# Kernel tuning notes

Hardware: AMD Instinct MI355X
Metric: run time of the kernel (lower is better)

Reference implementation:

```python
import jax, jax.numpy as jnp
import numpy as np

EMBED = 1024
HEADS = 16

def setup_inputs() -> dict:
    key = jax.random.key(0)
    ks = jax.random.split(key, 6)
    N, S = 1, 4096
    half = EMBED // 2
    x = jax.random.normal(ks[0], (N, S, EMBED), dtype=jnp.float32)
    Wq = jax.random.normal(ks[1], (half, half), dtype=jnp.float32) * 0.02
    Wk = jax.random.normal(ks[2], (half, half), dtype=jnp.float32) * 0.02
    Wv = jax.random.normal(ks[3], (half, half), dtype=jnp.float32) * 0.02
    Wo = jax.random.normal(ks[4], (EMBED, half), dtype=jnp.float32) * 0.02
    bo = jnp.zeros((EMBED,), dtype=jnp.float32)
    return {"x": x, "Wq": Wq, "Wk": Wk, "Wv": Wv, "Wo": Wo, "bo": bo}

def reference(x, Wq, Wk, Wv, Wo, bo):
    N, S, E = x.shape
    H = HEADS
    Dh = (E // 2) // H                 # per-head dim of the half-width projections (32)
    scale = float(E // H) ** 0.5       # original scales by head_dim = embed/heads = 64
    left = x[..., : E // 2]            # only the left chunk feeds attention in the source
    # torch Linear: y = x @ W.T (no bias)
    q = (left @ Wq.T).reshape(N, S, H, Dh)
    k = (left @ Wk.T).reshape(N, S, H, Dh)
    v = (left @ Wv.T).reshape(N, S, H, Dh)
    energy = jnp.einsum('nqhd,nkhd->nqkh', q, k)          # [N,S,S,H] full score tensor
    att = jax.nn.softmax(energy / scale, axis=2)          # softmax over key axis
    out = jnp.einsum('nqkh,nkhd->nqhd', att, v)           # [N,S,H,Dh]
    out = out.reshape(N, S, E // 2)
    return out @ Wo.T + bo                                # fc_out: half -> embed
```

## Files before the change

### kernel.cpp

```cpp
#include <hip/hip_runtime.h>
#include <stdint.h>


#define SEQ    4096
#define DMODEL 1024
#define DHALF  512
#define NH     16
#define DH     32

typedef __attribute__((ext_vector_type(4))) float facc4;
typedef __attribute__((ext_vector_type(8))) short bfrag8;

#define MFMA_BF16(a, b, c) __builtin_amdgcn_mfma_f32_16x16x32_bf16((a), (b), (c), 0, 0, 0)

static __device__ __forceinline__ uint16_t f2b(float x) {
    uint32_t u = __float_as_uint(x);
    return (uint16_t)((u + 0x7FFFu + ((u >> 16) & 1u)) >> 16);
}
static __device__ __forceinline__ float b2f(uint16_t b) {
    return __uint_as_float(((uint32_t)b) << 16);
}

static __device__ __forceinline__ bfrag8 cvt8perm(float4 a, float4 b) {
    uint32_t u0 = __float_as_uint(a.x) + 0x8000u, u1 = __float_as_uint(a.y) + 0x8000u;
    uint32_t u2 = __float_as_uint(a.z) + 0x8000u, u3 = __float_as_uint(a.w) + 0x8000u;
    uint32_t u4 = __float_as_uint(b.x) + 0x8000u, u5 = __float_as_uint(b.y) + 0x8000u;
    uint32_t u6 = __float_as_uint(b.z) + 0x8000u, u7 = __float_as_uint(b.w) + 0x8000u;
    union { uint32_t w[4]; bfrag8 r; } u;
    u.w[0] = __builtin_amdgcn_perm(u1, u0, 0x07060302u);
    u.w[1] = __builtin_amdgcn_perm(u3, u2, 0x07060302u);
    u.w[2] = __builtin_amdgcn_perm(u5, u4, 0x07060302u);
    u.w[3] = __builtin_amdgcn_perm(u7, u6, 0x07060302u);
    return u.r;
}

__global__ __launch_bounds__(256) void convert_w(
    const float* __restrict__ Wq, const float* __restrict__ Wk,
    const float* __restrict__ Wv, const float* __restrict__ Wo,
    uint16_t* __restrict__ q, uint16_t* __restrict__ k,
    uint16_t* __restrict__ v, uint16_t* __restrict__ o)
{
    int zz = blockIdx.x;
    const float* src; uint16_t* dst; size_t off;
    if      (zz < 128) { src = Wq; dst = q; off = (size_t)zz * 2048; }
    else if (zz < 256) { src = Wk; dst = k; off = (size_t)(zz - 128) * 2048; }
    else if (zz < 384) { src = Wv; dst = v; off = (size_t)(zz - 256) * 2048; }
    else               { src = Wo; dst = o; off = (size_t)(zz - 384) * 2048; }
    size_t i = off + (size_t)threadIdx.x * 8;
    float4 a = *(const float4*)&src[i];
    float4 b = *(const float4*)&src[i + 4];
    *(bfrag8*)&dst[i] = cvt8perm(a, b);
}

template <int AF32>
__device__ __forceinline__ void gemm128T(
    const void* __restrict__ A, int lda,
    const uint16_t* __restrict__ B, int ldb,
    void* __restrict__ C, int ldc, int cF32,
    const float* __restrict__ bias, float scale,
    int Kd, int m0, int n0)
{
    __shared__ __align__(16) uint16_t As[2][128 * 40];
    __shared__ __align__(16) uint16_t Bs[2][128 * 40];

    const int tid  = threadIdx.x;
    const int lane = tid & 63;
    const int wv   = tid >> 6;
    const int lo   = lane & 15;
    const int quad = lane >> 4;
    const int srow = tid >> 2;
    const int skq  = (tid & 3) * 8;
    const int rb   = (wv >> 1) * 64;
    const int cb   = (wv & 1) * 64;

    const facc4 ZACC = {0.f, 0.f, 0.f, 0.f};
    facc4 acc[4][4];
#pragma unroll
    for (int i = 0; i < 4; ++i)
#pragma unroll
        for (int j = 0; j < 4; ++j) acc[i][j] = ZACC;

    const float*    fA0 = AF32 ? &((const float*)A)[(size_t)(m0 + srow) * lda + skq] : nullptr;
    const float*    fA1 = AF32 ? &((const float*)A)[(size_t)(m0 + srow + 64) * lda + skq] : nullptr;
    const uint16_t* hA0 = AF32 ? nullptr : &((const uint16_t*)A)[(size_t)(m0 + srow) * lda + skq];
    const uint16_t* hA1 = AF32 ? nullptr : &((const uint16_t*)A)[(size_t)(m0 + srow + 64) * lda + skq];
    const uint16_t* pB0 = &B[(size_t)(n0 + srow) * ldb + skq];
    const uint16_t* pB1 = &B[(size_t)(n0 + srow + 64) * ldb + skq];

    bfrag8 ra0, ra1;
    float4 f0a, f0b, f1a, f1b;
    if (AF32) {
        f0a = *(const float4*)fA0; f0b = *(const float4*)(fA0 + 4);
        f1a = *(const float4*)fA1; f1b = *(const float4*)(fA1 + 4);
    } else {
        ra0 = *(const bfrag8*)hA0;
        ra1 = *(const bfrag8*)hA1;
    }
    bfrag8 rb0 = *(const bfrag8*)pB0;
    bfrag8 rb1 = *(const bfrag8*)pB1;

    if (AF32) {
        *(bfrag8*)&As[0][srow * 40 + skq]        = cvt8perm(f0a, f0b);
        *(bfrag8*)&As[0][(srow + 64) * 40 + skq] = cvt8perm(f1a, f1b);
    } else {
        *(bfrag8*)&As[0][srow * 40 + skq]        = ra0;
        *(bfrag8*)&As[0][(srow + 64) * 40 + skq] = ra1;
    }
    *(bfrag8*)&Bs[0][srow * 40 + skq]        = rb0;
    *(bfrag8*)&Bs[0][(srow + 64) * 40 + skq] = rb1;
    __syncthreads();

    int p = 0;
    for (int kt = 0; kt < Kd; kt += 32) {
        const bool more = (kt + 32 < Kd);
        if (more) {
            if (AF32) {
                f0a = *(const float4*)(fA0 + kt + 32); f0b = *(const float4*)(fA0 + kt + 36);
                f1a = *(const float4*)(fA1 + kt + 32); f1b = *(const float4*)(fA1 + kt + 36);
            } else {
                ra0 = *(const bfrag8*)(hA0 + kt + 32);
                ra1 = *(const bfrag8*)(hA1 + kt + 32);
            }
            rb0 = *(const bfrag8*)(pB0 + kt + 32);
            rb1 = *(const bfrag8*)(pB1 + kt + 32);
        }

        bfrag8 af[4], bf[4];
#pragma unroll
        for (int i = 0; i < 4; ++i) {
            af[i] = *(const bfrag8*)&As[p][(rb + i * 16 + lo) * 40 + quad * 8];
            bf[i] = *(const bfrag8*)&Bs[p][(cb + i * 16 + lo) * 40 + quad * 8];
        }
#pragma unroll
        for (int i = 0; i < 4; ++i)
#pragma unroll
            for (int j = 0; j < 4; ++j)
                acc[i][j] = MFMA_BF16(af[i], bf[j], acc[i][j]);

        if (more) {
            if (AF32) {
                *(bfrag8*)&As[1 - p][srow * 40 + skq]        = cvt8perm(f0a, f0b);
                *(bfrag8*)&As[1 - p][(srow + 64) * 40 + skq] = cvt8perm(f1a, f1b);
            } else {
                *(bfrag8*)&As[1 - p][srow * 40 + skq]        = ra0;
                *(bfrag8*)&As[1 - p][(srow + 64) * 40 + skq] = ra1;
            }
            *(bfrag8*)&Bs[1 - p][srow * 40 + skq]        = rb0;
            *(bfrag8*)&Bs[1 - p][(srow + 64) * 40 + skq] = rb1;
            __syncthreads();
            p ^= 1;
        }
    }

#pragma unroll
    for (int j = 0; j < 4; ++j) {
        int col  = n0 + cb + j * 16 + lo;
        float bv = bias ? bias[col] : 0.f;
#pragma unroll
        for (int i = 0; i < 4; ++i) {
#pragma unroll
            for (int r = 0; r < 4; ++r) {
                int row = m0 + rb + i * 16 + quad * 4 + r;
                float v = acc[i][j][r] * scale + bv;
                if (cF32) ((float*)C)[(size_t)row * ldc + col] = v;
                else      ((uint16_t*)C)[(size_t)row * ldc + col] = f2b(v);
            }
        }
    }
}

#define SC_Q (0.125f * 1.4426950408889634f)

__global__ __launch_bounds__(256, 2) void qkv_kernel(
    const float* __restrict__ x,
    const uint16_t* __restrict__ Wqb, const uint16_t* __restrict__ Wkb,
    const uint16_t* __restrict__ Wvb,
    uint16_t* __restrict__ Q, uint16_t* __restrict__ K, uint16_t* __restrict__ V)
{
    const int z = blockIdx.z;
    const uint16_t* W = (z == 0) ? Wqb : (z == 1) ? Wkb : Wvb;
    uint16_t* Out     = (z == 0) ? Q   : (z == 1) ? K   : V;
    float scale       = (z == 0) ? SC_Q : 1.0f;
    gemm128T<1>(x, DMODEL, W, DHALF, Out, DHALF, 0, nullptr, scale, DHALF,
                blockIdx.y * 128, blockIdx.x * 128);
}

__global__ __launch_bounds__(256, 2) void outproj_kernel(
    const uint16_t* __restrict__ O, const uint16_t* __restrict__ Wob,
    const float* __restrict__ bo, float* __restrict__ Y)
{
    gemm128T<0>(O, DHALF, Wob, DHALF, Y, DMODEL, 1, bo, 1.0f, DHALF,
                blockIdx.y * 128, blockIdx.x * 128);
}

__global__ __launch_bounds__(256) void attn_kernel(
    const uint16_t* __restrict__ Q, const uint16_t* __restrict__ Kb,
    const uint16_t* __restrict__ Vb, uint16_t* __restrict__ Op,
    float* __restrict__ lbuf, int kspan)
{
    __shared__ __align__(16) uint16_t Ks[64 * 40];
    __shared__ __align__(16) uint16_t Vt[32 * 64];
    __shared__ __align__(16) uint16_t Ps[4 * 16 * 72];

    const int tid  = threadIdx.x;
    const int lane = tid & 63;
    const int wv   = tid >> 6;
    const int lo   = lane & 15;
    const int quad = lane >> 4;
    const int h    = blockIdx.y;
    const int q0   = blockIdx.x * 64;
    const int sp   = blockIdx.z;
    const int srow = tid >> 2;
    const int skq  = (tid & 3) * 8;

    const facc4 ZACC = {0.f, 0.f, 0.f, 0.f};

    const bfrag8 qf = *(const bfrag8*)&Q[(size_t)(q0 + wv * 16 + lo) * DHALF + h * DH + quad * 8];

    bfrag8 ones;
#pragma unroll
    for (int j = 0; j < 8; ++j) ones[j] = (short)0x3F80;

    int vt_w[8];
#pragma unroll
    for (int j = 0; j < 8; ++j) {
        int d  = skq + j;
        int Rd = ((d & 7) + 2 * (d >> 3)) & 7;
        vt_w[j] = d * 64 + ((((srow >> 3) + Rd) & 7) << 3) + (srow & 7);
    }
    int vt_r[2][2];
#pragma unroll
    for (int dt = 0; dt < 2; ++dt) {
        int d  = dt * 16 + lo;
        int Rd = ((d & 7) + 2 * (d >> 3)) & 7;
#pragma unroll
        for (int c = 0; c < 2; ++c)
            vt_r[c][dt] = d * 64 + ((((c * 4 + quad) + Rd) & 7) << 3);
    }
    const int pbase = wv * (16 * 72);
    const int ps_w  = pbase + lo * 72 + 4 * quad;
    const int ps_r  = pbase + lo * 72 + quad * 8;
    const int ks_r  = lo * 40 + quad * 8;

    const uint16_t* pK = &Kb[(size_t)srow * DHALF + h * DH + skq];
    const uint16_t* pV = &Vb[(size_t)srow * DHALF + h * DH + skq];

    facc4 oacc[2], oaccL;
    oacc[0] = ZACC; oacc[1] = ZACC; oaccL = ZACC;

    const int kb0  = sp * kspan;
    const int kend = kb0 + kspan;

    float4 kreg = *(const float4*)(pK + (size_t)kb0 * DHALF);
    float4 vreg = *(const float4*)(pV + (size_t)kb0 * DHALF);

    for (int kb = kb0; kb < kend; kb += 64) {
        *(float4*)&Ks[srow * 40 + skq] = kreg;
        {
            const uint16_t* vp = (const uint16_t*)&vreg;
#pragma unroll
            for (int j = 0; j < 8; ++j) Vt[vt_w[j]] = vp[j];
        }
        __syncthreads();

        if (kb + 64 < kend) {
            kreg = *(const float4*)(pK + (size_t)(kb + 64) * DHALF);
            vreg = *(const float4*)(pV + (size_t)(kb + 64) * DHALF);
        }

#pragma unroll
        for (int t = 0; t < 4; ++t) {
            bfrag8 kf = *(const bfrag8*)&Ks[t * 640 + ks_r];
            facc4 s = MFMA_BF16(kf, qf, ZACC);
            float p0 = __builtin_amdgcn_exp2f(s[0]);
            float p1 = __builtin_amdgcn_exp2f(s[1]);
            float p2 = __builtin_amdgcn_exp2f(s[2]);
            float p3 = __builtin_amdgcn_exp2f(s[3]);
            uint32_t u0 = __float_as_uint(p0) + 0x8000u;
            uint32_t u1 = __float_as_uint(p1) + 0x8000u;
            uint32_t u2 = __float_as_uint(p2) + 0x8000u;
            uint32_t u3 = __float_as_uint(p3) + 0x8000u;
            uint2 w;
            w.x = __builtin_amdgcn_perm(u1, u0, 0x07060302u);
            w.y = __builtin_amdgcn_perm(u3, u2, 0x07060302u);
            *(uint2*)&Ps[ps_w + 16 * t] = w;
        }
        __builtin_amdgcn_wave_barrier();

#pragma unroll
        for (int c = 0; c < 2; ++c) {
            bfrag8 pf = *(const bfrag8*)&Ps[ps_r + c * 32];
#pragma unroll
            for (int dt = 0; dt < 2; ++dt) {
                bfrag8 vf = *(const bfrag8*)&Vt[vt_r[c][dt]];
                oacc[dt] = MFMA_BF16(pf, vf, oacc[dt]);
            }
            oaccL = MFMA_BF16(pf, ones, oaccL);
        }
        __syncthreads();
    }

    if (lo == 0) {
#pragma unroll
        for (int r = 0; r < 4; ++r)
            lbuf[((size_t)sp * NH + h) * SEQ + q0 + wv * 16 + quad * 4 + r] = oaccL[r];
    }

    uint16_t* Od = Op + (size_t)sp * SEQ * DHALF;
#pragma unroll
    for (int r = 0; r < 4; ++r) {
        int row = q0 + wv * 16 + quad * 4 + r;
        Od[(size_t)row * DHALF + h * DH + lo]      = f2b(oacc[0][r]);
        Od[(size_t)row * DHALF + h * DH + 16 + lo] = f2b(oacc[1][r]);
    }
}

__global__ __launch_bounds__(256) void combine_kernel(
    const uint16_t* __restrict__ Op, const float* __restrict__ lbuf,
    uint16_t* __restrict__ O, int ns)
{
    int t   = blockIdx.x * 256 + threadIdx.x;
    int row = t >> 6;
    int cb  = (t & 63) << 3;
    int h   = cb >> 5;
    float l = 0.f;
    float acc[8] = {0.f, 0.f, 0.f, 0.f, 0.f, 0.f, 0.f, 0.f};
    for (int sp = 0; sp < ns; ++sp) {
        l += lbuf[((size_t)sp * NH + h) * SEQ + row];
        bfrag8 a = *(const bfrag8*)&Op[(size_t)sp * SEQ * DHALF + (size_t)row * DHALF + cb];
#pragma unroll
        for (int j = 0; j < 8; ++j) acc[j] += b2f((uint16_t)a[j]);
    }
    float inv = 1.0f / l;
    bfrag8 o;
#pragma unroll
    for (int j = 0; j < 8; ++j) o[j] = (short)f2b(acc[j] * inv);
    *(bfrag8*)&O[(size_t)row * DHALF + cb] = o;
}

extern "C" void kernel_launch(void* const* d_in, const int* in_sizes, int n_in,
                              void* d_out, int out_size, void* d_ws, size_t ws_size,
                              hipStream_t stream)
{
    const float* x  = (const float*)d_in[0];
    const float* Wq = (const float*)d_in[1];
    const float* Wk = (const float*)d_in[2];
    const float* Wv = (const float*)d_in[3];
    const float* Wo = (const float*)d_in[4];
    const float* bo = (const float*)d_in[5];

    size_t fixed_e = 3 * (size_t)DHALF * DHALF + (size_t)DMODEL * DHALF
                   + 4 * (size_t)SEQ * DHALF;
    size_t need4 = (fixed_e + 4 * (size_t)SEQ * DHALF) * 2
                 + 4 * (size_t)NH * SEQ * 4;
    const int ns = (ws_size >= need4) ? 4 : 2;

    uint16_t* Wqb = (uint16_t*)d_ws;
    uint16_t* Wkb = Wqb + (size_t)DHALF * DHALF;
    uint16_t* Wvb = Wkb + (size_t)DHALF * DHALF;
    uint16_t* Wob = Wvb + (size_t)DHALF * DHALF;
    uint16_t* Q   = Wob + (size_t)DMODEL * DHALF;
    uint16_t* K   = Q + (size_t)SEQ * DHALF;
    uint16_t* V   = K + (size_t)SEQ * DHALF;
    uint16_t* O   = V + (size_t)SEQ * DHALF;
    uint16_t* Op  = O + (size_t)SEQ * DHALF;
    float*  lbuf  = (float*)(Op + (size_t)ns * SEQ * DHALF);

    convert_w<<<640, 256, 0, stream>>>(Wq, Wk, Wv, Wo, Wqb, Wkb, Wvb, Wob);
    qkv_kernel<<<dim3(DHALF / 128, SEQ / 128, 3), 256, 0, stream>>>(
        x, Wqb, Wkb, Wvb, Q, K, V);
    attn_kernel<<<dim3(SEQ / 64, NH, ns), 256, 0, stream>>>(Q, K, V, Op, lbuf, SEQ / ns);
    combine_kernel<<<1024, 256, 0, stream>>>(Op, lbuf, O, ns);
    outproj_kernel<<<dim3(DMODEL / 128, SEQ / 128), 256, 0, stream>>>(
        O, Wob, bo, (float*)d_out);
}
```

Baseline: 198.0 us.

## Double-buffer K/V tiles and keep P in registers via permuted V layout

The attention loop now keeps two LDS buffers for K and V tiles and writes the next tile after computing on the current one. This cuts the loop from two __syncthreads per iteration to one. The P matrix is no longer round-tripped through shared memory; it goes straight from the score MFMA output registers into the PV MFMA operand. To make that valid, the key-row order in the transposed V tile is permuted to match the register layout. This saves LDS traffic and a wave barrier, at the cost of twice the K/V LDS footprint and more delicate index math.

After: 189.0 us. 4.6% less time.

```diff
diff --git a/kernel.cpp b/kernel.cpp
--- a/kernel.cpp
+++ b/kernel.cpp
@@ -198,9 +198,8 @@
     const uint16_t* __restrict__ Vb, uint16_t* __restrict__ Op,
     float* __restrict__ lbuf, int kspan)
 {
-    __shared__ __align__(16) uint16_t Ks[64 * 40];
-    __shared__ __align__(16) uint16_t Vt[32 * 64];
-    __shared__ __align__(16) uint16_t Ps[4 * 16 * 72];
+    __shared__ __align__(16) uint16_t Ks[2][64 * 40];
+    __shared__ __align__(16) uint16_t Vt[2][32 * 64];
 
     const int tid  = threadIdx.x;
     const int lane = tid & 63;
@@ -222,11 +221,15 @@
     for (int j = 0; j < 8; ++j) ones[j] = (short)0x3F80;
 
     int vt_w[8];
-#pragma unroll
-    for (int j = 0; j < 8; ++j) {
-        int d  = skq + j;
-        int Rd = ((d & 7) + 2 * (d >> 3)) & 7;
-        vt_w[j] = d * 64 + ((((srow >> 3) + Rd) & 7) << 3) + (srow & 7);
+    {
+        int pb = ((srow >> 5) << 2) | ((srow >> 2) & 3);
+        int pw = (((srow >> 4) & 1) << 2) | (srow & 3);
+#pragma unroll
+        for (int j = 0; j < 8; ++j) {
+            int d  = skq + j;
+            int Rd = ((d & 7) + 2 * (d >> 3)) & 7;
+            vt_w[j] = d * 64 + (((pb + Rd) & 7) << 3) + pw;
+        }
     }
     int vt_r[2][2];
 #pragma unroll
@@ -237,10 +240,7 @@
         for (int c = 0; c < 2; ++c)
             vt_r[c][dt] = d * 64 + ((((c * 4 + quad) + Rd) & 7) << 3);
     }
-    const int pbase = wv * (16 * 72);
-    const int ps_w  = pbase + lo * 72 + 4 * quad;
-    const int ps_r  = pbase + lo * 72 + quad * 8;
-    const int ks_r  = lo * 40 + quad * 8;
+    const int ks_r = lo * 40 + quad * 8;
 
     const uint16_t* pK = &Kb[(size_t)srow * DHALF + h * DH + skq];
     const uint16_t* pV = &Vb[(size_t)srow * DHALF + h * DH + skq];
@@ -254,23 +254,26 @@
     float4 kreg = *(const float4*)(pK + (size_t)kb0 * DHALF);
     float4 vreg = *(const float4*)(pV + (size_t)kb0 * DHALF);
 
+    *(float4*)&Ks[0][srow * 40 + skq] = kreg;
+    {
+        const uint16_t* vp = (const uint16_t*)&vreg;
+#pragma unroll
+        for (int j = 0; j < 8; ++j) Vt[0][vt_w[j]] = vp[j];
+    }
+    __syncthreads();
+
+    int p = 0;
     for (int kb = kb0; kb < kend; kb += 64) {
-        *(float4*)&Ks[srow * 40 + skq] = kreg;
-        {
-            const uint16_t* vp = (const uint16_t*)&vreg;
-#pragma unroll
-            for (int j = 0; j < 8; ++j) Vt[vt_w[j]] = vp[j];
-        }
-        __syncthreads();
-
-        if (kb + 64 < kend) {
+        const bool more = (kb + 64 < kend);
+        if (more) {
             kreg = *(const float4*)(pK + (size_t)(kb + 64) * DHALF);
             vreg = *(const float4*)(pV + (size_t)(kb + 64) * DHALF);
         }
 
+        uint2 w[4];
 #pragma unroll
         for (int t = 0; t < 4; ++t) {
-            bfrag8 kf = *(const bfrag8*)&Ks[t * 640 + ks_r];
+            bfrag8 kf = *(const bfrag8*)&Ks[p][t * 640 + ks_r];
             facc4 s = MFMA_BF16(kf, qf, ZACC);
             float p0 = __builtin_amdgcn_exp2f(s[0]);
             float p1 = __builtin_amdgcn_exp2f(s[1]);
@@ -280,24 +283,34 @@
             uint32_t u1 = __float_as_uint(p1) + 0x8000u;
             uint32_t u2 = __float_as_uint(p2) + 0x8000u;
             uint32_t u3 = __float_as_uint(p3) + 0x8000u;
-            uint2 w;
-            w.x = __builtin_amdgcn_perm(u1, u0, 0x07060302u);
-            w.y = __builtin_amdgcn_perm(u3, u2, 0x07060302u);
-            *(uint2*)&Ps[ps_w + 16 * t] = w;
-        }
-        __builtin_amdgcn_wave_barrier();
+            w[t].x = __builtin_amdgcn_perm(u1, u0, 0x07060302u);
+            w[t].y = __builtin_amdgcn_perm(u3, u2, 0x07060302u);
+        }
+
+        union PU { uint2 u2[2]; bfrag8 f; };
+        PU pu0, pu1;
+        pu0.u2[0] = w[0]; pu0.u2[1] = w[1];
+        pu1.u2[0] = w[2]; pu1.u2[1] = w[3];
 
 #pragma unroll
         for (int c = 0; c < 2; ++c) {
-            bfrag8 pf = *(const bfrag8*)&Ps[ps_r + c * 32];
+            bfrag8 pf = c ? pu1.f : pu0.f;
 #pragma unroll
             for (int dt = 0; dt < 2; ++dt) {
-                bfrag8 vf = *(const bfrag8*)&Vt[vt_r[c][dt]];
+                bfrag8 vf = *(const bfrag8*)&Vt[p][vt_r[c][dt]];
                 oacc[dt] = MFMA_BF16(pf, vf, oacc[dt]);
             }
             oaccL = MFMA_BF16(pf, ones, oaccL);
         }
-        __syncthreads();
+
+        if (more) {
+            *(float4*)&Ks[p ^ 1][srow * 40 + skq] = kreg;
+            const uint16_t* vp = (const uint16_t*)&vreg;
+#pragma unroll
+            for (int j = 0; j < 8; ++j) Vt[p ^ 1][vt_w[j]] = vp[j];
+            __syncthreads();
+            p ^= 1;
+        }
     }
 
     if (lo == 0) {
```
